# Kernel tuning notes

Measured on AMD Instinct MI355X. Metric: run time of the kernel, lower is better.

The kernel has to match this reference:

```python
import jax, jax.numpy as jnp
import numpy as np

B, T, C, HS = 8, 2048, 1024, 64

def setup_inputs() -> dict:
    key = jax.random.key(0)
    ks = jax.random.split(key, 6)
    return {
        "q_vec": jax.random.normal(ks[0], (B, T, C), dtype=jnp.float32),
        "k_vec": jax.random.normal(ks[1], (B, T, C), dtype=jnp.float32),
        "v_vec": jax.random.normal(ks[2], (B, T, C), dtype=jnp.float32),
        "mask": jnp.ones((B, T), dtype=jnp.int32),
        "Wq": jax.random.normal(ks[3], (C, HS), dtype=jnp.float32) * (C ** -0.5),
        "Wk": jax.random.normal(ks[4], (C, HS), dtype=jnp.float32) * (C ** -0.5),
        "Wv": jax.random.normal(ks[5], (C, HS), dtype=jnp.float32) * (C ** -0.5),
    }

def reference(q_vec, k_vec, v_vec, mask, Wq, Wk, Wv):
    # bias-free linear projections: [B,T,C] @ [C,HS] -> [B,T,HS]
    q = jnp.einsum('btc,ch->bth', q_vec, Wq)
    k = jnp.einsum('btc,ch->bth', k_vec, Wk)
    v = jnp.einsum('btc,ch->bth', v_vec, Wv)
    scale = k.shape[-1] ** -0.5
    # full T x T score matrix, as in the original module
    scores = jnp.einsum('bth,bsh->bts', q, k) * scale  # [B,T,T]
    Tq = scores.shape[1]
    # _expand_along_time: expanded[b,i,j] = mask[b,j], then causal tril
    mask_exp = jnp.broadcast_to(mask[:, None, :].astype(jnp.float32), scores.shape)
    tril = jnp.tril(jnp.ones((Tq, Tq), dtype=jnp.float32))
    combined = mask_exp * tril[None, :, :]
    scores = jnp.where(combined == 0, -jnp.inf, scores)
    attn = jax.nn.softmax(scores, axis=-1)
    # dropout p=0.0 (eval) -> identity
    out = jnp.einsum('bts,bsh->bth', attn, v)  # [B,T,HS]
    return out
```

## Files before the change

kernel.cpp:

```cpp
#include <hip/hip_runtime.h>
#include <hip/hip_bf16.h>
#include <cmath>
#include <stdint.h>

#define B_ 8
#define T_ 2048
#define C_ 1024
#define HS_ 64
#define NS 8
#define LP 72
#define KCH 256
#define XLP 264

typedef __attribute__((ext_vector_type(8))) short short8;
typedef __attribute__((ext_vector_type(4))) float floatx4;

__device__ inline unsigned short f2bf(float f) {
    union { float f; unsigned u; } v; v.f = f;
    unsigned r = v.u + 0x7FFF + ((v.u >> 16) & 1);
    return (unsigned short)(r >> 16);
}
__device__ inline unsigned pk2bf(float a, float b) {
    union { __hip_bfloat162 h; unsigned u; } v;
    v.h = __float22bfloat162_rn(float2{a, b});
    return v.u;
}
__device__ inline float bf2f(unsigned short u) {
    union { unsigned u; float f; } w; w.u = ((unsigned)u) << 16; return w.f;
}

__global__ __launch_bounds__(256) void prep_wt(const float* __restrict__ Wq,
                                               const float* __restrict__ Wk,
                                               const float* __restrict__ Wv,
                                               unsigned short* __restrict__ wt) {
    int p = blockIdx.x >> 4;
    int chunk = blockIdx.x & 15;
    const float* W = (p == 0) ? Wq : (p == 1) ? Wk : Wv;
    unsigned short* WT = wt + p * (C_ * HS_);
    int base = chunk * 4096;
    for (int i = threadIdx.x; i < 4096; i += 256) {
        int idx = base + i;
        int k = idx >> 6, n = idx & 63;
        WT[n * C_ + k] = f2bf(W[idx]);
    }
}

__global__ __launch_bounds__(256) void proj_kernel(
    const float* __restrict__ qv, const float* __restrict__ kv, const float* __restrict__ vv,
    const unsigned short* __restrict__ wt,
    unsigned short* __restrict__ qb, unsigned short* __restrict__ kb, unsigned short* __restrict__ vb)
{
    __shared__ unsigned short Xl[64 * XLP];

    const int bid  = blockIdx.x;
    const int p    = bid >> 8;
    const int tile = bid & 255;
    const float* X = (p == 0) ? qv : (p == 1) ? kv : vv;
    const unsigned short* WT = wt + p * (C_ * HS_);
    unsigned short* Ob = (p == 0) ? qb : (p == 1) ? kb : vb;
    const float oscale = (p == 0) ? 0.125f : 1.0f;

    const int tid = threadIdx.x;
    const int wave = tid >> 6, lane = tid & 63, quad = lane >> 4, l16 = lane & 15;
    const long rowbase = (long)tile * 64;

    floatx4 acc[4] = { {0,0,0,0},{0,0,0,0},{0,0,0,0},{0,0,0,0} };

    const int srow = tid >> 5;
    const int sc8  = (tid & 31) * 8;

    for (int kc = 0; kc < C_; kc += KCH) {
        #pragma unroll
        for (int r8 = 0; r8 < 8; ++r8) {
            int row = r8 * 8 + srow;
            const float* gp = X + (rowbase + row) * C_ + kc + sc8;
            floatx4 f0 = *(const floatx4*)gp;
            floatx4 f1 = *(const floatx4*)(gp + 4);
            union { short8 s; unsigned u[4]; } a;
            a.u[0] = pk2bf(f0[0], f0[1]); a.u[1] = pk2bf(f0[2], f0[3]);
            a.u[2] = pk2bf(f1[0], f1[1]); a.u[3] = pk2bf(f1[2], f1[3]);
            *(short8*)&Xl[row * XLP + sc8] = a.s;
        }
        __syncthreads();

        #pragma unroll
        for (int kcc = 0; kcc < 8; ++kcc) {
            short8 af = *(short8*)&Xl[(wave * 16 + l16) * XLP + kcc * 32 + quad * 8];
            #pragma unroll
            for (int nt = 0; nt < 4; ++nt) {
                short8 bf = *(const short8*)&WT[(nt * 16 + l16) * C_ + kc + kcc * 32 + quad * 8];
                acc[nt] = __builtin_amdgcn_mfma_f32_16x16x32_bf16(af, bf, acc[nt], 0, 0, 0);
            }
        }
        __syncthreads();
    }

    #pragma unroll
    for (int nt = 0; nt < 4; ++nt)
        #pragma unroll
        for (int r = 0; r < 4; ++r) {
            long row = rowbase + wave * 16 + quad * 4 + r;
            Ob[row * HS_ + nt * 16 + l16] = f2bf(acc[nt][r] * oscale);
        }
}

__global__ __launch_bounds__(256) void attn_partial(
    const unsigned short* __restrict__ qb, const unsigned short* __restrict__ kb,
    const unsigned short* __restrict__ vb, const int* __restrict__ mask,
    unsigned short* __restrict__ Opart, float* __restrict__ Mpart, float* __restrict__ Lpart)
{
    const int s  = blockIdx.x & (NS - 1);
    const int bq = blockIdx.x >> 3;
    const int qt = bq & 31;
    const int b  = bq >> 5;
    if (s > qt) return;

    __shared__ unsigned short Klds[64 * LP];
    __shared__ unsigned short Vt[64 * LP];
    __shared__ unsigned short Plds[4][16 * LP];

    const int tid = threadIdx.x;
    const int wave = tid >> 6, lane = tid & 63, quad = lane >> 4, l16 = lane & 15;

    const int qrow = qt * 64 + wave * 16 + l16;
    const unsigned short* qp = qb + ((long)(b * T_ + qrow)) * HS_;
    short8 aq0 = *(const short8*)&qp[0  + quad * 8];
    short8 aq1 = *(const short8*)&qp[32 + quad * 8];

    floatx4 acc_o[4] = { {0,0,0,0},{0,0,0,0},{0,0,0,0},{0,0,0,0} };
    float m_r[4] = { -INFINITY, -INFINITY, -INFINITY, -INFINITY };
    float l_r[4] = { 0.f, 0.f, 0.f, 0.f };

    const int rowg = qt * 64 + wave * 16 + quad * 4;

    const int skey = tid >> 3;
    const int sf8  = (tid & 7) * 8;
    const int vp = tid & 31, vg = tid >> 5;

    for (int c = s; c <= qt; c += NS) {
        const int kc = c * 64;
        #pragma unroll
        for (int it = 0; it < 2; ++it) {
            int key = it * 32 + skey;
            *(short8*)&Klds[key * LP + sf8] =
                *(const short8*)&kb[((long)(b * T_ + kc + key)) * HS_ + sf8];
        }
        {
            const unsigned short* v0p = &vb[((long)(b * T_ + kc + 2 * vp)) * HS_ + vg * 8];
            short8 v0 = *(const short8*)v0p;
            short8 v1 = *(const short8*)(v0p + HS_);
            #pragma unroll
            for (int j = 0; j < 8; ++j) {
                unsigned pr = (unsigned)(unsigned short)v0[j] |
                              ((unsigned)(unsigned short)v1[j] << 16);
                *(unsigned*)&Vt[(vg * 8 + j) * LP + 2 * vp] = pr;
            }
        }
        __syncthreads();

        floatx4 sv[4];
        #pragma unroll
        for (int kt = 0; kt < 4; ++kt) {
            floatx4 a = {0.f, 0.f, 0.f, 0.f};
            short8 bk0 = *(short8*)&Klds[(kt * 16 + l16) * LP + 0  + quad * 8];
            short8 bk1 = *(short8*)&Klds[(kt * 16 + l16) * LP + 32 + quad * 8];
            a = __builtin_amdgcn_mfma_f32_16x16x32_bf16(aq0, bk0, a, 0, 0, 0);
            a = __builtin_amdgcn_mfma_f32_16x16x32_bf16(aq1, bk1, a, 0, 0, 0);
            sv[kt] = a;
        }

        const bool lastc = (c == qt);
        #pragma unroll
        for (int kt = 0; kt < 4; ++kt) {
            int key = kc + kt * 16 + l16;
            int mk = mask[b * T_ + key];
            #pragma unroll
            for (int r = 0; r < 4; ++r) {
                bool dead = (mk == 0) || (lastc && key > rowg + r);
                if (dead) sv[kt][r] = -INFINITY;
            }
        }

        float alpha[4];
        #pragma unroll
        for (int r = 0; r < 4; ++r) {
            float mx = fmaxf(fmaxf(sv[0][r], sv[1][r]), fmaxf(sv[2][r], sv[3][r]));
            #pragma unroll
            for (int off = 1; off < 16; off <<= 1)
                mx = fmaxf(mx, __shfl_xor(mx, off));
            float mn = fmaxf(m_r[r], mx);
            float a_ = __expf(m_r[r] - mn);
            float ps = 0.f;
            #pragma unroll
            for (int kt = 0; kt < 4; ++kt) {
                float pv = __expf(sv[kt][r] - mn);
                sv[kt][r] = pv;
                ps += pv;
            }
            #pragma unroll
            for (int off = 1; off < 16; off <<= 1)
                ps += __shfl_xor(ps, off);
            l_r[r] = l_r[r] * a_ + ps;
            m_r[r] = mn;
            alpha[r] = a_;
        }
        #pragma unroll
        for (int nt = 0; nt < 4; ++nt)
            #pragma unroll
            for (int r = 0; r < 4; ++r)
                acc_o[nt][r] *= alpha[r];

        unsigned short* pl = Plds[wave];
        #pragma unroll
        for (int kt = 0; kt < 4; ++kt)
            #pragma unroll
            for (int r = 0; r < 4; ++r)
                pl[(quad * 4 + r) * LP + kt * 16 + l16] = f2bf(sv[kt][r]);
        short8 ap0 = *(short8*)&pl[l16 * LP + 0  + quad * 8];
        short8 ap1 = *(short8*)&pl[l16 * LP + 32 + quad * 8];

        #pragma unroll
        for (int nt = 0; nt < 4; ++nt) {
            short8 bv0 = *(short8*)&Vt[(nt * 16 + l16) * LP + 0  + quad * 8];
            short8 bv1 = *(short8*)&Vt[(nt * 16 + l16) * LP + 32 + quad * 8];
            acc_o[nt] = __builtin_amdgcn_mfma_f32_16x16x32_bf16(ap0, bv0, acc_o[nt], 0, 0, 0);
            acc_o[nt] = __builtin_amdgcn_mfma_f32_16x16x32_bf16(ap1, bv1, acc_o[nt], 0, 0, 0);
        }
        __syncthreads();
    }

    unsigned short* Op = Opart + (long)blockIdx.x * 4096;
    #pragma unroll
    for (int nt = 0; nt < 4; ++nt)
        #pragma unroll
        for (int r = 0; r < 4; ++r)
            Op[(wave * 16 + quad * 4 + r) * 64 + nt * 16 + l16] = f2bf(acc_o[nt][r]);
    if (l16 == 0) {
        #pragma unroll
        for (int r = 0; r < 4; ++r) {
            int rl = wave * 16 + quad * 4 + r;
            Mpart[(long)blockIdx.x * 64 + rl] = m_r[r];
            Lpart[(long)blockIdx.x * 64 + rl] = l_r[r];
        }
    }
}

__global__ __launch_bounds__(256) void attn_combine(
    const unsigned short* __restrict__ Opart, const float* __restrict__ Mpart,
    const float* __restrict__ Lpart, float* __restrict__ out)
{
    const int half = blockIdx.x & 1;
    const int bq = blockIdx.x >> 1;
    const int qt = bq & 31;
    const int b  = bq >> 5;
    const int nsp = (qt + 1 < NS) ? qt + 1 : NS;

    const int row  = (threadIdx.x >> 3) + half * 32;
    const int colg = (threadIdx.x & 7) * 8;
    const long base = (long)bq * NS;

    float M = -INFINITY;
    #pragma unroll
    for (int sp = 0; sp < NS; ++sp)
        if (sp < nsp) M = fmaxf(M, Mpart[(base + sp) * 64 + row]);

    float w[NS];
    float L = 0.f;
    #pragma unroll
    for (int sp = 0; sp < NS; ++sp)
        if (sp < nsp) {
            float e = __expf(Mpart[(base + sp) * 64 + row] - M);
            w[sp] = e;
            L += e * Lpart[(base + sp) * 64 + row];
        }

    float acc[8] = {0,0,0,0,0,0,0,0};
    #pragma unroll
    for (int sp = 0; sp < NS; ++sp)
        if (sp < nsp) {
            const unsigned short* Op = Opart + (base + sp) * 4096 + row * 64 + colg;
            short8 o = *(const short8*)Op;
            float ws = w[sp];
            #pragma unroll
            for (int j = 0; j < 8; ++j)
                acc[j] += ws * bf2f((unsigned short)o[j]);
        }

    float inv = 1.0f / L;
    float* op = out + ((long)(b * T_ + qt * 64 + row)) * HS_ + colg;
    floatx4 o0 = { acc[0] * inv, acc[1] * inv, acc[2] * inv, acc[3] * inv };
    floatx4 o1 = { acc[4] * inv, acc[5] * inv, acc[6] * inv, acc[7] * inv };
    *(floatx4*)op = o0;
    *(floatx4*)(op + 4) = o1;
}

extern "C" void kernel_launch(void* const* d_in, const int* in_sizes, int n_in,
                              void* d_out, int out_size, void* d_ws, size_t ws_size,
                              hipStream_t stream)
{
    const float* qv = (const float*)d_in[0];
    const float* kv = (const float*)d_in[1];
    const float* vv = (const float*)d_in[2];
    const int*   mask = (const int*)d_in[3];
    const float* Wq = (const float*)d_in[4];
    const float* Wk = (const float*)d_in[5];
    const float* Wv = (const float*)d_in[6];
    float* out = (float*)d_out;

    unsigned short* wt    = (unsigned short*)d_ws;
    unsigned short* qbuf  = wt + 3 * C_ * HS_;
    unsigned short* kbuf  = qbuf + (long)B_ * T_ * HS_;
    unsigned short* vbuf  = kbuf + (long)B_ * T_ * HS_;
    unsigned short* Opart = vbuf + (long)B_ * T_ * HS_;
    float* Mpart = (float*)(Opart + (long)B_ * 32 * NS * 4096);
    float* Lpart = Mpart + (long)B_ * 32 * NS * 64;

    prep_wt<<<48, 256, 0, stream>>>(Wq, Wk, Wv, wt);
    proj_kernel<<<768, 256, 0, stream>>>(qv, kv, vv, wt, qbuf, kbuf, vbuf);
    attn_partial<<<B_ * 32 * NS, 256, 0, stream>>>(qbuf, kbuf, vbuf, mask, Opart, Mpart, Lpart);
    attn_combine<<<B_ * 32 * 2, 256, 0, stream>>>(Opart, Mpart, Lpart, out);
}
```

Baseline: 291.1 us.

## Prefetch next projection chunk into registers and stage weights in LDS

The projection kernel now loads the next 128-wide K chunk of X and the bf16 weights into registers while MFMAs run on the current chunk in LDS. This is a software-pipelined register prefetch. Weights are also staged in shared memory instead of being read from global memory inside the MFMA loop. The chunk size is halved and launch bounds request 4 blocks per CU for more occupancy. This costs extra registers and doubles the number of sync iterations.

```diff
diff --git a/kernel.cpp b/kernel.cpp
--- a/kernel.cpp
+++ b/kernel.cpp
@@ -9,8 +9,8 @@
 #define HS_ 64
 #define NS 8
 #define LP 72
-#define KCH 256
-#define XLP 264
+#define PKC 128
+#define XLP2 136
 
 typedef __attribute__((ext_vector_type(8))) short short8;
 typedef __attribute__((ext_vector_type(4))) float floatx4;
@@ -45,12 +45,13 @@
     }
 }
 
-__global__ __launch_bounds__(256) void proj_kernel(
+__global__ __launch_bounds__(256, 4) void proj_kernel(
     const float* __restrict__ qv, const float* __restrict__ kv, const float* __restrict__ vv,
     const unsigned short* __restrict__ wt,
     unsigned short* __restrict__ qb, unsigned short* __restrict__ kb, unsigned short* __restrict__ vb)
 {
-    __shared__ unsigned short Xl[64 * XLP];
+    __shared__ unsigned short Xl[64 * XLP2];
+    __shared__ unsigned short Wl[64 * XLP2];
 
     const int bid  = blockIdx.x;
     const int p    = bid >> 8;
@@ -63,32 +64,55 @@
     const int tid = threadIdx.x;
     const int wave = tid >> 6, lane = tid & 63, quad = lane >> 4, l16 = lane & 15;
     const long rowbase = (long)tile * 64;
+    const float* Xbase = X + rowbase * C_;
+
+    const int xsub = lane & 31;
+    const int xrp  = lane >> 5;
+    const int wsub = lane & 15;
+    const int wr4  = lane >> 4;
+
+    floatx4 xf[8];
+    short8  wf[4];
+
+    #pragma unroll
+    for (int i = 0; i < 8; ++i)
+        xf[i] = *(const floatx4*)(Xbase + (wave * 16 + i * 2 + xrp) * C_ + xsub * 4);
+    #pragma unroll
+    for (int i = 0; i < 4; ++i)
+        wf[i] = *(const short8*)(WT + (wave * 16 + i * 4 + wr4) * C_ + wsub * 8);
 
     floatx4 acc[4] = { {0,0,0,0},{0,0,0,0},{0,0,0,0},{0,0,0,0} };
 
-    const int srow = tid >> 5;
-    const int sc8  = (tid & 31) * 8;
-
-    for (int kc = 0; kc < C_; kc += KCH) {
-        #pragma unroll
-        for (int r8 = 0; r8 < 8; ++r8) {
-            int row = r8 * 8 + srow;
-            const float* gp = X + (rowbase + row) * C_ + kc + sc8;
-            floatx4 f0 = *(const floatx4*)gp;
-            floatx4 f1 = *(const floatx4*)(gp + 4);
-            union { short8 s; unsigned u[4]; } a;
-            a.u[0] = pk2bf(f0[0], f0[1]); a.u[1] = pk2bf(f0[2], f0[3]);
-            a.u[2] = pk2bf(f1[0], f1[1]); a.u[3] = pk2bf(f1[2], f1[3]);
-            *(short8*)&Xl[row * XLP + sc8] = a.s;
-        }
+    for (int c = 0; c < C_ / PKC; ++c) {
+        #pragma unroll
+        for (int i = 0; i < 8; ++i) {
+            int row = wave * 16 + i * 2 + xrp;
+            unsigned u0 = pk2bf(xf[i][0], xf[i][1]);
+            unsigned u1 = pk2bf(xf[i][2], xf[i][3]);
+            unsigned* d = (unsigned*)&Xl[row * XLP2 + xsub * 4];
+            d[0] = u0; d[1] = u1;
+        }
+        #pragma unroll
+        for (int i = 0; i < 4; ++i)
+            *(short8*)&Wl[(wave * 16 + i * 4 + wr4) * XLP2 + wsub * 8] = wf[i];
         __syncthreads();
 
-        #pragma unroll
-        for (int kcc = 0; kcc < 8; ++kcc) {
-            short8 af = *(short8*)&Xl[(wave * 16 + l16) * XLP + kcc * 32 + quad * 8];
+        if (c + 1 < C_ / PKC) {
+            const int kc = (c + 1) * PKC;
+            #pragma unroll
+            for (int i = 0; i < 8; ++i)
+                xf[i] = *(const floatx4*)(Xbase + (wave * 16 + i * 2 + xrp) * C_ + kc + xsub * 4);
+            #pragma unroll
+            for (int i = 0; i < 4; ++i)
+                wf[i] = *(const short8*)(WT + (wave * 16 + i * 4 + wr4) * C_ + kc + wsub * 8);
+        }
+
+        #pragma unroll
+        for (int kcc = 0; kcc < 4; ++kcc) {
+            short8 af = *(short8*)&Xl[(wave * 16 + l16) * XLP2 + kcc * 32 + quad * 8];
             #pragma unroll
             for (int nt = 0; nt < 4; ++nt) {
-                short8 bf = *(const short8*)&WT[(nt * 16 + l16) * C_ + kc + kcc * 32 + quad * 8];
+                short8 bf = *(short8*)&Wl[(nt * 16 + l16) * XLP2 + kcc * 32 + quad * 8];
                 acc[nt] = __builtin_amdgcn_mfma_f32_16x16x32_bf16(af, bf, acc[nt], 0, 0, 0);
             }
         }
```

Result: faster. 260.4 us (-10.6%).

## Stage projection inputs and weights via direct global-to-LDS loads with XOR swizzle

Applied to the files above, without the earlier changes.

The projection kernel now copies fp32 X tiles and bf16 weight tiles straight into shared memory with global_load_lds in 64-wide K chunks, using XOR-swizzled layouts. The fp32-to-bf16 conversion moves to after the LDS read, and weights are now read from LDS rather than from global memory. The aim is to cut register-staged copies and repeated global weight loads. In exchange there are more chunk iterations with a barrier pair each, and there is still no double buffering, so load latency stays exposed.

```diff
diff --git a/kernel.cpp b/kernel.cpp
--- a/kernel.cpp
+++ b/kernel.cpp
@@ -9,8 +9,6 @@
 #define HS_ 64
 #define NS 8
 #define LP 72
-#define KCH 256
-#define XLP 264
 
 typedef __attribute__((ext_vector_type(8))) short short8;
 typedef __attribute__((ext_vector_type(4))) float floatx4;
@@ -27,6 +25,12 @@
 }
 __device__ inline float bf2f(unsigned short u) {
     union { unsigned u; float f; } w; w.u = ((unsigned)u) << 16; return w.f;
+}
+__device__ inline void gl2lds16(const void* g, void* l) {
+    __builtin_amdgcn_global_load_lds(
+        (const __attribute__((address_space(1))) unsigned int*)g,
+        (__attribute__((address_space(3))) unsigned int*)l,
+        16, 0, 0);
 }
 
 __global__ __launch_bounds__(256) void prep_wt(const float* __restrict__ Wq,
@@ -50,7 +54,8 @@
     const unsigned short* __restrict__ wt,
     unsigned short* __restrict__ qb, unsigned short* __restrict__ kb, unsigned short* __restrict__ vb)
 {
-    __shared__ unsigned short Xl[64 * XLP];
+    __shared__ __align__(16) float Xl[64 * 64];
+    __shared__ __align__(16) unsigned short Wl[64 * 64];
 
     const int bid  = blockIdx.x;
     const int p    = bid >> 8;
@@ -63,33 +68,47 @@
     const int tid = threadIdx.x;
     const int wave = tid >> 6, lane = tid & 63, quad = lane >> 4, l16 = lane & 15;
     const long rowbase = (long)tile * 64;
+    const float* Xbase = X + rowbase * C_;
+
+    const int xrow_l = lane >> 4, xblk = lane & 15;
+    const int wrow_l = lane >> 3, wblk = lane & 7;
 
     floatx4 acc[4] = { {0,0,0,0},{0,0,0,0},{0,0,0,0},{0,0,0,0} };
 
-    const int srow = tid >> 5;
-    const int sc8  = (tid & 31) * 8;
-
-    for (int kc = 0; kc < C_; kc += KCH) {
-        #pragma unroll
-        for (int r8 = 0; r8 < 8; ++r8) {
-            int row = r8 * 8 + srow;
-            const float* gp = X + (rowbase + row) * C_ + kc + sc8;
-            floatx4 f0 = *(const floatx4*)gp;
-            floatx4 f1 = *(const floatx4*)(gp + 4);
-            union { short8 s; unsigned u[4]; } a;
-            a.u[0] = pk2bf(f0[0], f0[1]); a.u[1] = pk2bf(f0[2], f0[3]);
-            a.u[2] = pk2bf(f1[0], f1[1]); a.u[3] = pk2bf(f1[2], f1[3]);
-            *(short8*)&Xl[row * XLP + sc8] = a.s;
+    for (int c = 0; c < 16; ++c) {
+        const int kc = c * 64;
+        #pragma unroll
+        for (int ii = 0; ii < 4; ++ii) {
+            int i = wave * 4 + ii;
+            int row = i * 4 + xrow_l;
+            const float* src = Xbase + (long)row * C_ + kc + ((xblk ^ (row & 15)) * 4);
+            gl2lds16(src, &Xl[i * 256]);
+        }
+        #pragma unroll
+        for (int jj = 0; jj < 2; ++jj) {
+            int j = wave * 2 + jj;
+            int row = j * 8 + wrow_l;
+            const unsigned short* src = WT + row * C_ + kc + ((wblk ^ (row & 7)) * 8);
+            gl2lds16(src, &Wl[j * 512]);
         }
         __syncthreads();
 
         #pragma unroll
-        for (int kcc = 0; kcc < 8; ++kcc) {
-            short8 af = *(short8*)&Xl[(wave * 16 + l16) * XLP + kcc * 32 + quad * 8];
+        for (int ks = 0; ks < 2; ++ks) {
+            const int xrow = wave * 16 + l16;
+            int lb = (ks * 8 + 2 * quad) ^ l16;
+            const float* xr = &Xl[xrow * 64];
+            floatx4 flo = *(const floatx4*)(xr + lb * 4);
+            floatx4 fhi = *(const floatx4*)(xr + (lb ^ 1) * 4);
+            union { short8 s8; unsigned u[4]; } af;
+            af.u[0] = pk2bf(flo[0], flo[1]); af.u[1] = pk2bf(flo[2], flo[3]);
+            af.u[2] = pk2bf(fhi[0], fhi[1]); af.u[3] = pk2bf(fhi[2], fhi[3]);
             #pragma unroll
             for (int nt = 0; nt < 4; ++nt) {
-                short8 bf = *(const short8*)&WT[(nt * 16 + l16) * C_ + kc + kcc * 32 + quad * 8];
-                acc[nt] = __builtin_amdgcn_mfma_f32_16x16x32_bf16(af, bf, acc[nt], 0, 0, 0);
+                int wrow = nt * 16 + l16;
+                int wb = (ks * 4 + quad) ^ (l16 & 7);
+                short8 bf = *(const short8*)&Wl[wrow * 64 + wb * 8];
+                acc[nt] = __builtin_amdgcn_mfma_f32_16x16x32_bf16(af.s8, bf, acc[nt], 0, 0, 0);
             }
         }
         __syncthreads();
```

Measured after the change: 267.2 us. -8.2%, faster.
